# Kernel tuning notes

Measured on AMD Instinct MI355X. Metric: run time of the kernel, lower is better.

The kernel has to match this reference:

```python
import jax, jax.numpy as jnp
import numpy as np

B, S, H = 2, 256, 256
R = H  # rdim defaults to hidden_size


def setup_inputs() -> dict:
    key = jax.random.key(0)
    k1, k2, k3 = jax.random.split(key, 3)
    hidden_states = jax.random.normal(k1, (B, S, H), dtype=jnp.float32)
    # Linear weights stored torch-style [out, in]
    Wqkv = jax.random.normal(k2, (3 * R, H), dtype=jnp.float32) * (H ** -0.5)
    bqkv = jnp.zeros((3 * R,), dtype=jnp.float32)
    Wc = jax.random.normal(k3, (R, R), dtype=jnp.float32) * (R ** -0.5)
    bc = jnp.zeros((R,), dtype=jnp.float32)
    return {"hidden_states": hidden_states, "Wqkv": Wqkv, "bqkv": bqkv, "Wc": Wc, "bc": bc}


def reference(hidden_states, Wqkv, bqkv, Wc, bc):
    # qkv projection: [B,S,3R]
    qkv = jnp.einsum('bsh,rh->bsr', hidden_states, Wqkv) + bqkv
    q, k, v = jnp.split(qkv, 3, axis=-1)  # each [B,S,R]
    # Tucker-style outer-product scores: [B,S,L,R]
    scores = jnp.einsum('bsr,blr->bslr', q, k)
    # c_proj mixes the r dimension
    scores = jnp.einsum('bslr,pr->bslp', scores, Wc) + bc
    # rearrange 'b s l r -> (b r) s l' + softmax(dim=-1) == softmax over l axis
    probs = jax.nn.softmax(scores, axis=2)
    # 'brsl,blr->bsr' after rearrange back == 'bslr,blr->bsr'
    return jnp.einsum('bslr,blr->bsr', probs, v)
```

## Files before the change

kernel.cpp:

```cpp
#include <hip/hip_runtime.h>
#include <hip/hip_bf16.h>
#include <math.h>

typedef __bf16 bf16;
typedef _Float16 f16;
typedef __attribute__((ext_vector_type(8))) __bf16 bf16x8;
typedef __attribute__((ext_vector_type(8))) _Float16 f16x8;
typedef __attribute__((ext_vector_type(4))) _Float16 f16x4;
typedef __attribute__((ext_vector_type(4))) float floatx4;

__device__ __forceinline__ void split8(floatx4 a0, floatx4 a1, bf16x8& hi, bf16x8& lo) {
#pragma unroll
    for (int t = 0; t < 4; t++) {
        float v0 = a0[t], v1 = a1[t];
        bf16 h0 = (bf16)v0, h1 = (bf16)v1;
        hi[t] = h0;     lo[t] = (bf16)(v0 - (float)h0);
        hi[t + 4] = h1; lo[t + 4] = (bf16)(v1 - (float)h1);
    }
}

__global__ __launch_bounds__(256, 4)
void proj_kernel(const float* __restrict__ hs, const float* __restrict__ Wq,
                 const float* __restrict__ bq, const float* __restrict__ Wc,
                 f16* __restrict__ q_ws, f16* __restrict__ k_ws,
                 f16* __restrict__ vT_ws, f16* __restrict__ Wc_ws)
{
    const int tid = threadIdx.x;
    if (blockIdx.x >= 384) {
        const int base = (blockIdx.x - 384) * 1024 + tid * 4;
        floatx4 w = *(const floatx4*)(Wc + base);
        f16x4 h;
        h.x = (f16)w.x; h.y = (f16)w.y; h.z = (f16)w.z; h.w = (f16)w.w;
        *(f16x4*)(Wc_ws + base) = h;
        return;
    }
    const int wv = tid >> 6, lane = tid & 63;
    const int quad = lane >> 4, lcol = lane & 15;
    const int wt = blockIdx.x * 4 + wv;
    const int rt = wt / 48, ct = wt - rt * 48;
    const int row0 = rt * 16, col0 = ct * 16;

    const float* arow = hs + (row0 + lcol) * 256;
    const float* brow = Wq + (col0 + lcol) * 256;

    floatx4 acc = {0.f, 0.f, 0.f, 0.f};
#pragma unroll
    for (int ks = 0; ks < 8; ks++) {
        const int h = ks * 32 + quad * 8;
        floatx4 a0 = *(const floatx4*)(arow + h);
        floatx4 a1 = *(const floatx4*)(arow + h + 4);
        floatx4 b0 = *(const floatx4*)(brow + h);
        floatx4 b1 = *(const floatx4*)(brow + h + 4);
        bf16x8 ahi, alo, bhi, blo;
        split8(a0, a1, ahi, alo);
        split8(b0, b1, bhi, blo);
        acc = __builtin_amdgcn_mfma_f32_16x16x32_bf16(ahi, bhi, acc, 0, 0, 0);
        acc = __builtin_amdgcn_mfma_f32_16x16x32_bf16(ahi, blo, acc, 0, 0, 0);
        acc = __builtin_amdgcn_mfma_f32_16x16x32_bf16(alo, bhi, acc, 0, 0, 0);
    }
    const float bias = bq[col0 + lcol];
    const int col = col0 + lcol, seg = col0 >> 8, jj = col & 255;
#pragma unroll
    for (int r = 0; r < 4; r++) {
        const int row = row0 + quad * 4 + r;
        const float val = acc[r] + bias;
        if (seg == 0)      q_ws[row * 256 + jj] = (f16)val;
        else if (seg == 1) k_ws[row * 256 + jj] = (f16)val;
        else               vT_ws[(row >> 8) * 65536 + jj * 256 + (row & 255)] = (f16)val;
    }
}

__global__ __launch_bounds__(512, 2)
void attn_partial(const f16* __restrict__ qw, const f16* __restrict__ kw,
                  const f16* __restrict__ vT, const f16* __restrict__ Wc16,
                  float* __restrict__ osum_ws, float* __restrict__ ssum_ws)
{
    __shared__ f16 Klds[64 * 256];
    __shared__ f16 Wlds[64 * 256];
    __shared__ f16 vTlds[64 * 68];

    const int bid = blockIdx.x;
    const int pt = bid & 3;
    const int lq = (bid >> 2) & 3;
    const int sg = (bid >> 4) & 31;
    const int b  = bid >> 9;
    const int p0 = pt * 64;
    const int l0 = lq * 64;
    const int tid  = threadIdx.x;
    const int wv   = tid >> 6;
    const int lane = tid & 63;
    const int quad = lane >> 4, lcol = lane & 15;
    const int ph = wv & 1, lh = (wv >> 1) & 1, sp = wv >> 2;
    const int s_base = sg * 8 + sp * 4;

    const f16* kbase = kw + b * 65536;
    const f16* vbase = vT + b * 65536;
    const f16* qbase = qw + (b * 256 + s_base) * 256;

#pragma unroll
    for (int it = 0; it < 4; it++) {
        const int id = it * 512 + tid;
        const int r = id >> 5, c = id & 31;
        const int csrc = c ^ (r & 7);
        *(uint4*)(Klds + r * 256 + c * 8) =
            *(const uint4*)(kbase + (l0 + r) * 256 + csrc * 8);
    }
#pragma unroll
    for (int it = 0; it < 4; it++) {
        const int id = it * 512 + tid;
        const int r = id >> 5, c = id & 31;
        const int csrc = c ^ (r & 7);
        *(uint4*)(Wlds + r * 256 + c * 8) =
            *(const uint4*)(Wc16 + (p0 + r) * 256 + csrc * 8);
    }
#pragma unroll
    for (int it = 0; it < 2; it++) {
        const int id = it * 512 + tid;
        const int p = id >> 4, c = id & 15;
        *(f16x4*)(vTlds + p * 68 + c * 4) =
            *(const f16x4*)(vbase + (p0 + p) * 256 + l0 + c * 4);
    }
    __syncthreads();

    floatx4 acc[4][2][2];
#pragma unroll
    for (int u = 0; u < 4; u++)
#pragma unroll
        for (int i = 0; i < 2; i++)
#pragma unroll
            for (int j = 0; j < 2; j++)
                acc[u][i][j] = (floatx4){0.f, 0.f, 0.f, 0.f};

#pragma unroll
    for (int kk = 0; kk < 8; kk++) {
        const int rb = kk * 32 + quad * 8;
        const int sw = ((kk * 4 + quad) ^ (lcol & 7)) << 3;
        f16x8 qv[4];
#pragma unroll
        for (int u = 0; u < 4; u++)
            qv[u] = *(const f16x8*)(qbase + u * 256 + rb);
        f16x8 kf[2];
#pragma unroll
        for (int i = 0; i < 2; i++)
            kf[i] = *(const f16x8*)(Klds + (lh * 32 + i * 16 + lcol) * 256 + sw);
        f16x8 w8[2];
#pragma unroll
        for (int j = 0; j < 2; j++)
            w8[j] = *(const f16x8*)(Wlds + (ph * 32 + j * 16 + lcol) * 256 + sw);
#pragma unroll
        for (int u = 0; u < 4; u++) {
#pragma unroll
            for (int j = 0; j < 2; j++) {
                f16x8 bfr = w8[j] * qv[u];
#pragma unroll
                for (int i = 0; i < 2; i++)
                    acc[u][i][j] = __builtin_amdgcn_mfma_f32_16x16x32_f16(kf[i], bfr, acc[u][i][j], 0, 0, 0);
            }
        }
    }

    float os[4][2] = {{0.f,0.f},{0.f,0.f},{0.f,0.f},{0.f,0.f}};
    float ss[4][2] = {{0.f,0.f},{0.f,0.f},{0.f,0.f},{0.f,0.f}};
#pragma unroll
    for (int i = 0; i < 2; i++) {
#pragma unroll
        for (int j = 0; j < 2; j++) {
            f16x4 vf = *(const f16x4*)(vTlds + (ph * 32 + j * 16 + lcol) * 68 + lh * 32 + i * 16 + quad * 4);
            const float vF0 = (float)vf[0], vF1 = (float)vf[1], vF2 = (float)vf[2], vF3 = (float)vf[3];
#pragma unroll
            for (int u = 0; u < 4; u++) {
                const float P0 = __expf(acc[u][i][j][0]);
                const float P1 = __expf(acc[u][i][j][1]);
                const float P2 = __expf(acc[u][i][j][2]);
                const float P3 = __expf(acc[u][i][j][3]);
                os[u][j] = fmaf(P0, vF0, os[u][j]);
                os[u][j] = fmaf(P1, vF1, os[u][j]);
                os[u][j] = fmaf(P2, vF2, os[u][j]);
                os[u][j] = fmaf(P3, vF3, os[u][j]);
                ss[u][j] += (P0 + P1) + (P2 + P3);
            }
        }
    }

#pragma unroll
    for (int u = 0; u < 4; u++)
#pragma unroll
        for (int j = 0; j < 2; j++) {
            os[u][j] += __shfl_xor(os[u][j], 16);
            os[u][j] += __shfl_xor(os[u][j], 32);
            ss[u][j] += __shfl_xor(ss[u][j], 16);
            ss[u][j] += __shfl_xor(ss[u][j], 32);
        }
    if (quad == 0) {
#pragma unroll
        for (int u = 0; u < 4; u++) {
            const int base = ((b * 256 + s_base + u) * 8 + lq * 2 + lh) * 256 + p0 + ph * 32;
#pragma unroll
            for (int j = 0; j < 2; j++) {
                osum_ws[base + j * 16 + lcol] = os[u][j];
                ssum_ws[base + j * 16 + lcol] = ss[u][j];
            }
        }
    }
}

__global__ __launch_bounds__(256, 4)
void merge_kernel(const float* __restrict__ osum_ws, const float* __restrict__ ssum_ws,
                  float* __restrict__ out)
{
    const int g = blockIdx.x * 256 + threadIdx.x;
    const int p = g & 255, bs = g >> 8;
    const int base = bs * 2048 + p;
    float O = 0.f, S = 0.f;
#pragma unroll
    for (int sl = 0; sl < 8; sl++) {
        O += osum_ws[base + sl * 256];
        S += ssum_ws[base + sl * 256];
    }
    out[g] = O / S;
}

extern "C" void kernel_launch(void* const* d_in, const int* in_sizes, int n_in,
                              void* d_out, int out_size, void* d_ws, size_t ws_size,
                              hipStream_t stream) {
    const float* hs   = (const float*)d_in[0];
    const float* Wqkv = (const float*)d_in[1];
    const float* bqkv = (const float*)d_in[2];
    const float* Wc   = (const float*)d_in[3];
    float* out = (float*)d_out;

    char* ws = (char*)d_ws;
    f16* q_ws   = (f16*)ws;
    f16* k_ws   = (f16*)(ws + 262144);
    f16* vT_ws  = (f16*)(ws + 524288);
    f16* Wc_ws  = (f16*)(ws + 786432);
    float* osum_ws = (float*)(ws + 1048576);
    float* ssum_ws = (float*)(ws + 5242880);

    proj_kernel<<<dim3(448), 256, 0, stream>>>(hs, Wqkv, bqkv, Wc, q_ws, k_ws, vT_ws, Wc_ws);
    attn_partial<<<dim3(1024), 512, 0, stream>>>(q_ws, k_ws, vT_ws, Wc_ws, osum_ws, ssum_ws);
    merge_kernel<<<dim3(512), 256, 0, stream>>>(osum_ws, ssum_ws, out);
}
```

Measured before the change: 106.0 us.

## Remap attention waves to cover full 64-l tile with two s rows each

Changes the per-wave work split in attn_partial: each wave now handles all 64 l values of the block's tile (4 K fragments) for 2 s rows, instead of 32 l values for 4 s rows. This halves the per-wave q loads and elementwise Wc*q products relative to MFMA count, and halves the partial-sum workspace, since partials no longer need the extra lh split. The merge kernel now sums 4 partials instead of 8. The trade-off is more K LDS reads per wave.

Result: faster. 90.42 us (-14.7%).

```diff
diff --git a/kernel.cpp b/kernel.cpp
--- a/kernel.cpp
+++ b/kernel.cpp
@@ -90,8 +90,8 @@
     const int wv   = tid >> 6;
     const int lane = tid & 63;
     const int quad = lane >> 4, lcol = lane & 15;
-    const int ph = wv & 1, lh = (wv >> 1) & 1, sp = wv >> 2;
-    const int s_base = sg * 8 + sp * 4;
+    const int ph = wv & 1, sp = wv >> 1;
+    const int s_base = sg * 8 + sp * 2;
 
     const f16* kbase = kw + b * 65536;
     const f16* vbase = vT + b * 65536;
@@ -122,11 +122,11 @@
     }
     __syncthreads();
 
-    floatx4 acc[4][2][2];
-#pragma unroll
-    for (int u = 0; u < 4; u++)
-#pragma unroll
-        for (int i = 0; i < 2; i++)
+    floatx4 acc[2][4][2];
+#pragma unroll
+    for (int u = 0; u < 2; u++)
+#pragma unroll
+        for (int i = 0; i < 4; i++)
 #pragma unroll
             for (int j = 0; j < 2; j++)
                 acc[u][i][j] = (floatx4){0.f, 0.f, 0.f, 0.f};
@@ -135,40 +135,38 @@
     for (int kk = 0; kk < 8; kk++) {
         const int rb = kk * 32 + quad * 8;
         const int sw = ((kk * 4 + quad) ^ (lcol & 7)) << 3;
-        f16x8 qv[4];
-#pragma unroll
-        for (int u = 0; u < 4; u++)
-            qv[u] = *(const f16x8*)(qbase + u * 256 + rb);
-        f16x8 kf[2];
-#pragma unroll
-        for (int i = 0; i < 2; i++)
-            kf[i] = *(const f16x8*)(Klds + (lh * 32 + i * 16 + lcol) * 256 + sw);
+        f16x8 qv0 = *(const f16x8*)(qbase + rb);
+        f16x8 qv1 = *(const f16x8*)(qbase + 256 + rb);
+        f16x8 kf[4];
+#pragma unroll
+        for (int i = 0; i < 4; i++)
+            kf[i] = *(const f16x8*)(Klds + (i * 16 + lcol) * 256 + sw);
         f16x8 w8[2];
 #pragma unroll
         for (int j = 0; j < 2; j++)
             w8[j] = *(const f16x8*)(Wlds + (ph * 32 + j * 16 + lcol) * 256 + sw);
 #pragma unroll
-        for (int u = 0; u < 4; u++) {
-#pragma unroll
-            for (int j = 0; j < 2; j++) {
-                f16x8 bfr = w8[j] * qv[u];
-#pragma unroll
-                for (int i = 0; i < 2; i++)
-                    acc[u][i][j] = __builtin_amdgcn_mfma_f32_16x16x32_f16(kf[i], bfr, acc[u][i][j], 0, 0, 0);
+        for (int j = 0; j < 2; j++) {
+            f16x8 bf0 = w8[j] * qv0;
+            f16x8 bf1 = w8[j] * qv1;
+#pragma unroll
+            for (int i = 0; i < 4; i++) {
+                acc[0][i][j] = __builtin_amdgcn_mfma_f32_16x16x32_f16(kf[i], bf0, acc[0][i][j], 0, 0, 0);
+                acc[1][i][j] = __builtin_amdgcn_mfma_f32_16x16x32_f16(kf[i], bf1, acc[1][i][j], 0, 0, 0);
             }
         }
     }
 
-    float os[4][2] = {{0.f,0.f},{0.f,0.f},{0.f,0.f},{0.f,0.f}};
-    float ss[4][2] = {{0.f,0.f},{0.f,0.f},{0.f,0.f},{0.f,0.f}};
-#pragma unroll
-    for (int i = 0; i < 2; i++) {
+    float os[2][2] = {{0.f,0.f},{0.f,0.f}};
+    float ss[2][2] = {{0.f,0.f},{0.f,0.f}};
+#pragma unroll
+    for (int i = 0; i < 4; i++) {
 #pragma unroll
         for (int j = 0; j < 2; j++) {
-            f16x4 vf = *(const f16x4*)(vTlds + (ph * 32 + j * 16 + lcol) * 68 + lh * 32 + i * 16 + quad * 4);
+            f16x4 vf = *(const f16x4*)(vTlds + (ph * 32 + j * 16 + lcol) * 68 + i * 16 + quad * 4);
             const float vF0 = (float)vf[0], vF1 = (float)vf[1], vF2 = (float)vf[2], vF3 = (float)vf[3];
 #pragma unroll
-            for (int u = 0; u < 4; u++) {
+            for (int u = 0; u < 2; u++) {
                 const float P0 = __expf(acc[u][i][j][0]);
                 const float P1 = __expf(acc[u][i][j][1]);
                 const float P2 = __expf(acc[u][i][j][2]);
@@ -183,7 +181,7 @@
     }
 
 #pragma unroll
-    for (int u = 0; u < 4; u++)
+    for (int u = 0; u < 2; u++)
 #pragma unroll
         for (int j = 0; j < 2; j++) {
             os[u][j] += __shfl_xor(os[u][j], 16);
@@ -193,8 +191,8 @@
         }
     if (quad == 0) {
 #pragma unroll
-        for (int u = 0; u < 4; u++) {
-            const int base = ((b * 256 + s_base + u) * 8 + lq * 2 + lh) * 256 + p0 + ph * 32;
+        for (int u = 0; u < 2; u++) {
+            const int base = ((b * 256 + s_base + u) * 4 + lq) * 256 + p0 + ph * 32;
 #pragma unroll
             for (int j = 0; j < 2; j++) {
                 osum_ws[base + j * 16 + lcol] = os[u][j];
@@ -210,12 +208,12 @@
 {
     const int g = blockIdx.x * 256 + threadIdx.x;
     const int p = g & 255, bs = g >> 8;
-    const int base = bs * 2048 + p;
+    const int base = bs * 1024 + p;
     float O = 0.f, S = 0.f;
 #pragma unroll
-    for (int sl = 0; sl < 8; sl++) {
-        O += osum_ws[base + sl * 256];
-        S += ssum_ws[base + sl * 256];
+    for (int lq = 0; lq < 4; lq++) {
+        O += osum_ws[base + lq * 256];
+        S += ssum_ws[base + lq * 256];
     }
     out[g] = O / S;
 }
@@ -235,7 +233,7 @@
     f16* vT_ws  = (f16*)(ws + 524288);
     f16* Wc_ws  = (f16*)(ws + 786432);
     float* osum_ws = (float*)(ws + 1048576);
-    float* ssum_ws = (float*)(ws + 5242880);
+    float* ssum_ws = (float*)(ws + 3145728);
 
     proj_kernel<<<dim3(448), 256, 0, stream>>>(hs, Wqkv, bqkv, Wc, q_ws, k_ws, vT_ws, Wc_ws);
     attn_partial<<<dim3(1024), 512, 0, stream>>>(q_ws, k_ws, vT_ws, Wc_ws, osum_ws, ssum_ws);
```
